# Kernel optimization log

Hardware: AMD Instinct MI355X
Metric: run time of the kernel (lower is better)

## Reference

```python
import jax, jax.numpy as jnp
import numpy as np

B, L, C, H = 256, 200, 4, 128


def setup_inputs() -> dict:
    key = jax.random.key(0)
    ks = jax.random.split(key, 6)
    seqs = jax.random.normal(ks[0], (B, L, C, H), dtype=jnp.float32)
    # valid prefix of random length, padding (True) at the tail
    lengths = jax.random.randint(ks[1], (B,), 1, L + 1)
    timeline_mask = (jnp.arange(L)[None, :] >= lengths[:, None])[:, :, None]  # [B,L,1] bool
    attention_mask = jnp.zeros((L, L), dtype=bool)  # unused by the module
    s = 1.0 / np.sqrt(H)  # torch GRU default init U(-1/sqrt(H), 1/sqrt(H))
    W_ih = jax.random.uniform(ks[2], (C, 3 * H, H), minval=-s, maxval=s, dtype=jnp.float32)
    W_hh = jax.random.uniform(ks[3], (C, 3 * H, H), minval=-s, maxval=s, dtype=jnp.float32)
    b_ih = jax.random.uniform(ks[4], (C, 3 * H), minval=-s, maxval=s, dtype=jnp.float32)
    b_hh = jax.random.uniform(ks[5], (C, 3 * H), minval=-s, maxval=s, dtype=jnp.float32)
    return {"seqs": seqs, "timeline_mask": timeline_mask, "attention_mask": attention_mask,
            "W_ih": W_ih, "W_hh": W_hh, "b_ih": b_ih, "b_hh": b_hh}


def batched_roll(x, shifts):
    # x: [B, L, H]; per-sample circular shift along time (torch.roll semantics)
    Ldim = x.shape[1]
    idx = (jnp.arange(Ldim)[None, :] - shifts[:, None]) % Ldim  # [B, L]
    return jnp.take_along_axis(x, idx[:, :, None], axis=1)


def gru(x, W_ih, W_hh, b_ih, b_hh):
    # single-layer batch_first GRU, h0 = 0 (torch nn.GRU math)
    xp = jnp.einsum('blh,gh->blg', x, W_ih) + b_ih  # [B, L, 3H] input projections
    Hd = W_hh.shape[1]

    def step(h, xt):
        gh = h @ W_hh.T + b_hh
        i_r, i_z, i_n = jnp.split(xt, 3, axis=-1)
        h_r, h_z, h_n = jnp.split(gh, 3, axis=-1)
        r = jax.nn.sigmoid(i_r + h_r)
        z = jax.nn.sigmoid(i_z + h_z)
        n = jnp.tanh(i_n + r * h_n)
        h_new = (1.0 - z) * n + z * h
        return h_new, h_new

    h0 = jnp.zeros((x.shape[0], Hd), x.dtype)
    _, ys = jax.lax.scan(step, h0, jnp.swapaxes(xp, 0, 1))  # scan over time
    return jnp.swapaxes(ys, 0, 1)  # [B, L, H]


def reference(seqs, timeline_mask, attention_mask, W_ih, W_hh, b_ih, b_hh):
    mask = timeline_mask[:, :, 0]                 # [B, L] True = pad
    length = jnp.sum(~mask, axis=1)               # count of valid steps
    zero_length = jnp.sum(mask, axis=1)           # count of padded steps
    outs = []
    for i in range(seqs.shape[2]):                # loop over C experts (distinct weights)
        x = batched_roll(seqs[:, :, i, :], length)
        y = gru(x, W_ih[i], W_hh[i], b_ih[i], b_hh[i])
        y = batched_roll(y, zero_length)
        y = jnp.where(timeline_mask, 0.0, y)      # masked_fill(timeline_mask, 0.0)
        outs.append(y)
    return jnp.stack(outs, axis=0)  # [C, B, L, H] (list of experts in the original)
```

## Files before the change

kernel.cpp:

```cpp
#include <hip/hip_runtime.h>
#include <hip/hip_bf16.h>

#define BB 256
#define LL 200
#define CC 4
#define HH 128
#define G3 384
#define XPAD 168

typedef short bf16x8 __attribute__((ext_vector_type(8)));
typedef float f32x4 __attribute__((ext_vector_type(4)));

#define MFMA16(a, b, c) __builtin_amdgcn_mfma_f32_16x16x32_bf16((a), (b), (c), 0, 0, 0)

__device__ __forceinline__ short bf16_rne(float x) {
    union { float f; unsigned u; } v; v.f = x;
    unsigned r = v.u + 0x7FFFu + ((v.u >> 16) & 1u);
    return (short)(r >> 16);
}
__device__ __forceinline__ float rcp_(float x) { return __builtin_amdgcn_rcpf(x); }
__device__ __forceinline__ float sigm_(float x) { return rcp_(1.0f + __expf(-x)); }
__device__ __forceinline__ float tanhf_(float x) { return 2.0f * rcp_(1.0f + __expf(-2.0f * x)) - 1.0f; }

__device__ __forceinline__ unsigned cvtpk(float lo, float hi) {
    unsigned r;
    asm("v_cvt_pk_bf16_f32 %0, %1, %2" : "=v"(r) : "v"(lo), "v"(hi));
    return r;
}
__device__ __forceinline__ uint2 pack4(float4 v) {
    uint2 p;
    p.x = cvtpk(v.x, v.y);
    p.y = cvtpk(v.z, v.w);
    return p;
}

__global__ void compute_lens_kernel(const unsigned char* __restrict__ mask8,
                                    int* __restrict__ lens) {
    __shared__ int bad;
    int b = threadIdx.x;
    if (b == 0) bad = 0;
    __syncthreads();
    int cnt8 = 0, prev = 0, mono = 1;
    for (int t = 0; t < LL; ++t) {
        int v = mask8[b * LL + t] ? 1 : 0;
        cnt8 += (v == 0);
        if (v < prev) mono = 0;
        prev = v;
    }
    if (!mono) atomicAdd(&bad, 1);
    __syncthreads();
    int len;
    if (bad == 0) {
        len = cnt8;
    } else {
        const int* m32 = (const int*)mask8;
        int c = 0;
        for (int t = 0; t < LL; ++t) c += (m32[b * LL + t] == 0);
        len = c;
    }
    if (len < 1) len = 1;
    if (len > LL) len = LL;
    lens[b] = len;
}

__global__ void wsplit_kernel(const float* __restrict__ Wih, const float* __restrict__ Whh,
                              short* __restrict__ wih_hi, short* __restrict__ whh_hi) {
    int i = blockIdx.x * 256 + threadIdx.x;
    wih_hi[i] = bf16_rne(Wih[i]);
    whh_hi[i] = bf16_rne(Whh[i]);
}

__global__ __launch_bounds__(512, 2) void gru_fused_kernel(
    const float* __restrict__ seqs,
    const int*   __restrict__ lens,
    const short* __restrict__ wih_hi,
    const short* __restrict__ whh_hi,
    const float* __restrict__ b_ih,
    const float* __restrict__ b_hh,
    float*       __restrict__ out)
{
    const int bt = blockIdx.x;
    const int c  = blockIdx.y;
    const int bbase = bt * 16;
    const int tid = threadIdx.x;
    const int w = tid >> 6;
    const int l = tid & 63;
    const int l15 = l & 15, g = l >> 4;

    __shared__ __align__(16) short hA[2][16][XPAD];
    __shared__ __align__(16) short xs[2][16][XPAD];

    bf16x8 BH[3][4], WI[3][4];
    #pragma unroll
    for (int q = 0; q < 3; ++q) {
        const int NT = q * 8 + w;
        #pragma unroll
        for (int ks = 0; ks < 4; ++ks) {
            size_t off = (size_t)(c * G3 + NT * 16 + l15) * HH + ks * 32 + g * 8;
            BH[q][ks] = *(const bf16x8*)(whh_hi + off);
            WI[q][ks] = *(const bf16x8*)(wih_hi + off);
        }
    }
    #pragma unroll
    for (int q = 0; q < 3; ++q)
        asm volatile("" : "+a"(BH[q][0]), "+a"(BH[q][1]), "+a"(BH[q][2]), "+a"(BH[q][3]));

    const int bsl = tid >> 5;
    const int bs  = bbase + bsl;
    const int k0s = (tid & 31) * 4;
    const int lenS = lens[bs];
    const float* srow = seqs + ((size_t)bs * LL * CC + c) * HH + k0s;
    int ts0 = LL - lenS;
    int ts1 = ts0 + 1; if (ts1 >= LL) ts1 -= LL;
    float4 xr0 = *(const float4*)(srow + (size_t)ts0 * (CC * HH));
    float4 xr1 = *(const float4*)(srow + (size_t)ts1 * (CC * HH));
    int txs = ts1 + 1; if (txs >= LL) txs -= LL;

    const int col0 = w * 16 + l15;
    const float bRs = b_hh[c * G3 + col0]       + b_ih[c * G3 + col0];
    const float bZs = b_hh[c * G3 + 128 + col0] + b_ih[c * G3 + 128 + col0];
    const float bHN = b_hh[c * G3 + 256 + col0];
    const float bIN = b_ih[c * G3 + 256 + col0];
    const f32x4 cZZ  = (f32x4){0.f, 0.f, 0.f, 0.f};
    const f32x4 cHN4 = (f32x4){bHN, bHN, bHN, bHN};
    const f32x4 cR4  = (f32x4){bRs, bRs, bRs, bRs};
    const f32x4 cZ4  = (f32x4){bZs, bZs, bZs, bZs};
    const f32x4 cN4  = (f32x4){bIN, bIN, bIN, bIN};

    int lenr[4], tcur[4];
    #pragma unroll
    for (int r = 0; r < 4; ++r) {
        lenr[r] = lens[bbase + g * 4 + r];
        tcur[r] = LL - lenr[r];
    }
    float hold[4] = { 0.f, 0.f, 0.f, 0.f };

    for (int i = tid; i < 16 * XPAD / 2; i += 512) ((int*)hA[0])[i] = 0;

    *(uint2*)&xs[0][bsl][k0s] = pack4(xr0);
    *(uint2*)&xs[1][bsl][k0s] = pack4(xr1);
    __syncthreads();

    f32x4 xacc[3];
    {
        bf16x8 xh0 = *(const bf16x8*)&xs[0][l15][g * 8];
        xacc[0] = MFMA16(xh0, WI[0][0], cR4);
        xacc[1] = MFMA16(xh0, WI[1][0], cZ4);
        xacc[2] = MFMA16(xh0, WI[2][0], cN4);
        #pragma unroll
        for (int ks = 1; ks < 4; ++ks) {
            bf16x8 xh = *(const bf16x8*)&xs[0][l15][ks * 32 + g * 8];
            #pragma unroll
            for (int q = 0; q < 3; ++q)
                xacc[q] = MFMA16(xh, WI[q][ks], xacc[q]);
        }
    }
    float4 xraw = *(const float4*)(srow + (size_t)txs * (CC * HH));
    txs = (txs + 1 == LL) ? 0 : txs + 1;

    __syncthreads();

    for (int si = 0; si < LL; ++si) {
        const int hb = si & 1, hn = hb ^ 1;

        f32x4 racc[3];
        {
            bf16x8 ah0 = *(const bf16x8*)&hA[hb][l15][g * 8];
            racc[0] = MFMA16(ah0, BH[0][0], cZZ);
            racc[1] = MFMA16(ah0, BH[1][0], cZZ);
            racc[2] = MFMA16(ah0, BH[2][0], cHN4);
            #pragma unroll
            for (int ks = 1; ks < 4; ++ks) {
                bf16x8 ah = *(const bf16x8*)&hA[hb][l15][ks * 32 + g * 8];
                #pragma unroll
                for (int q = 0; q < 3; ++q) racc[q] = MFMA16(ah, BH[q][ks], racc[q]);
            }
        }

        float hnew[4];
        #pragma unroll
        for (int r = 0; r < 4; ++r) {
            float gr = sigm_(racc[0][r] + xacc[0][r]);
            float gz = sigm_(racc[1][r] + xacc[1][r]);
            float gn = tanhf_(xacc[2][r] + gr * racc[2][r]);
            float hv = gn + gz * (hold[r] - gn);
            hnew[r] = hv;
            hold[r] = hv;
        }

        {
            unsigned pk01 = cvtpk(hold[0], hold[1]);
            unsigned pk23 = cvtpk(hold[2], hold[3]);
            hA[hn][g * 4 + 0][col0] = (short)(pk01 & 0xffffu);
            hA[hn][g * 4 + 1][col0] = (short)(pk01 >> 16);
            hA[hn][g * 4 + 2][col0] = (short)(pk23 & 0xffffu);
            hA[hn][g * 4 + 3][col0] = (short)(pk23 >> 16);
        }

        #pragma unroll
        for (int r = 0; r < 4; ++r) {
            int t = tcur[r];
            int valid = t < lenr[r];
            out[((size_t)(c * BB + bbase + g * 4 + r) * LL + t) * HH + col0]
                = valid ? hnew[r] : 0.0f;
            tcur[r] = (t + 1 == LL) ? 0 : t + 1;
        }

        {
            bf16x8 xh0 = *(const bf16x8*)&xs[hn][l15][g * 8];
            xacc[0] = MFMA16(xh0, WI[0][0], cR4);
            xacc[1] = MFMA16(xh0, WI[1][0], cZ4);
            xacc[2] = MFMA16(xh0, WI[2][0], cN4);
            #pragma unroll
            for (int ks = 1; ks < 4; ++ks) {
                bf16x8 xh = *(const bf16x8*)&xs[hn][l15][ks * 32 + g * 8];
                #pragma unroll
                for (int q = 0; q < 3; ++q)
                    xacc[q] = MFMA16(xh, WI[q][ks], xacc[q]);
            }
        }

        *(uint2*)&xs[hb][bsl][k0s] = pack4(xraw);
        xraw = *(const float4*)(srow + (size_t)txs * (CC * HH));
        txs = (txs + 1 == LL) ? 0 : txs + 1;

        asm volatile("s_waitcnt lgkmcnt(0)" ::: "memory");
        __builtin_amdgcn_s_barrier();
        __builtin_amdgcn_sched_barrier(0);
        asm volatile("" ::: "memory");
    }
}

extern "C" void kernel_launch(void* const* d_in, const int* in_sizes, int n_in,
                              void* d_out, int out_size, void* d_ws, size_t ws_size,
                              hipStream_t stream) {
    const float* seqs  = (const float*)d_in[0];
    const unsigned char* tmask = (const unsigned char*)d_in[1];
    const float* W_ih  = (const float*)d_in[3];
    const float* W_hh  = (const float*)d_in[4];
    const float* b_ih  = (const float*)d_in[5];
    const float* b_hh  = (const float*)d_in[6];
    float* out = (float*)d_out;

    char* ws = (char*)d_ws;
    int*   lens   = (int*)(ws);
    short* wih_hi = (short*)(ws + 1024);
    short* whh_hi = (short*)(ws + 1024 + 393216);

    compute_lens_kernel<<<1, BB, 0, stream>>>(tmask, lens);
    wsplit_kernel<<<768, 256, 0, stream>>>(W_ih, W_hh, wih_hi, whh_hi);

    gru_fused_kernel<<<dim3(16, CC), 512, 0, stream>>>(
        seqs, lens, wih_hi, whh_hi, b_ih, b_hh, out);
}
```

Baseline: 203.6 us.

## Specialize warps into recurrent and input-projection roles with LDS handoff

```diff
diff --git a/kernel.cpp b/kernel.cpp
--- a/kernel.cpp
+++ b/kernel.cpp
@@ -26,12 +26,6 @@
     unsigned r;
     asm("v_cvt_pk_bf16_f32 %0, %1, %2" : "=v"(r) : "v"(lo), "v"(hi));
     return r;
-}
-__device__ __forceinline__ uint2 pack4(float4 v) {
-    uint2 p;
-    p.x = cvtpk(v.x, v.y);
-    p.y = cvtpk(v.z, v.w);
-    return p;
 }
 
 __global__ void compute_lens_kernel(const unsigned char* __restrict__ mask8,
@@ -86,144 +80,211 @@
     const int w = tid >> 6;
     const int l = tid & 63;
     const int l15 = l & 15, g = l >> 4;
+    const int role = w >> 2;
+    const int wq = w & 3;
 
     __shared__ __align__(16) short hA[2][16][XPAD];
     __shared__ __align__(16) short xs[2][16][XPAD];
-
-    bf16x8 BH[3][4], WI[3][4];
+    __shared__ __align__(16) float xp[G3][16];
+
+    bf16x8 W[6][4];
+    {
+        const short* wsrc = role ? wih_hi : whh_hi;
+        #pragma unroll
+        for (int q = 0; q < 6; ++q) {
+            const int NT = (q >> 1) * 8 + 2 * wq + (q & 1);
+            #pragma unroll
+            for (int ks = 0; ks < 4; ++ks) {
+                size_t off = (size_t)(c * G3 + NT * 16 + l15) * HH + ks * 32 + g * 8;
+                W[q][ks] = *(const bf16x8*)(wsrc + off);
+            }
+        }
+    }
     #pragma unroll
-    for (int q = 0; q < 3; ++q) {
-        const int NT = q * 8 + w;
-        #pragma unroll
-        for (int ks = 0; ks < 4; ++ks) {
-            size_t off = (size_t)(c * G3 + NT * 16 + l15) * HH + ks * 32 + g * 8;
-            BH[q][ks] = *(const bf16x8*)(whh_hi + off);
-            WI[q][ks] = *(const bf16x8*)(wih_hi + off);
-        }
-    }
-    #pragma unroll
-    for (int q = 0; q < 3; ++q)
-        asm volatile("" : "+a"(BH[q][0]), "+a"(BH[q][1]), "+a"(BH[q][2]), "+a"(BH[q][3]));
-
-    const int bsl = tid >> 5;
-    const int bs  = bbase + bsl;
-    const int k0s = (tid & 31) * 4;
-    const int lenS = lens[bs];
-    const float* srow = seqs + ((size_t)bs * LL * CC + c) * HH + k0s;
-    int ts0 = LL - lenS;
-    int ts1 = ts0 + 1; if (ts1 >= LL) ts1 -= LL;
-    float4 xr0 = *(const float4*)(srow + (size_t)ts0 * (CC * HH));
-    float4 xr1 = *(const float4*)(srow + (size_t)ts1 * (CC * HH));
-    int txs = ts1 + 1; if (txs >= LL) txs -= LL;
-
-    const int col0 = w * 16 + l15;
-    const float bRs = b_hh[c * G3 + col0]       + b_ih[c * G3 + col0];
-    const float bZs = b_hh[c * G3 + 128 + col0] + b_ih[c * G3 + 128 + col0];
-    const float bHN = b_hh[c * G3 + 256 + col0];
-    const float bIN = b_ih[c * G3 + 256 + col0];
-    const f32x4 cZZ  = (f32x4){0.f, 0.f, 0.f, 0.f};
-    const f32x4 cHN4 = (f32x4){bHN, bHN, bHN, bHN};
-    const f32x4 cR4  = (f32x4){bRs, bRs, bRs, bRs};
-    const f32x4 cZ4  = (f32x4){bZs, bZs, bZs, bZs};
-    const f32x4 cN4  = (f32x4){bIN, bIN, bIN, bIN};
+    for (int q = 0; q < 6; ++q)
+        asm volatile("" : "+a"(W[q][0]), "+a"(W[q][1]), "+a"(W[q][2]), "+a"(W[q][3]));
+
+    const int colA = 32 * wq + l15;
+    const int colB = colA + 16;
+
+    f32x4 ci[6];
+    if (role) {
+        float bRa = b_hh[c * G3 + colA]       + b_ih[c * G3 + colA];
+        float bRb = b_hh[c * G3 + colB]       + b_ih[c * G3 + colB];
+        float bZa = b_hh[c * G3 + 128 + colA] + b_ih[c * G3 + 128 + colA];
+        float bZb = b_hh[c * G3 + 128 + colB] + b_ih[c * G3 + 128 + colB];
+        float bNa = b_ih[c * G3 + 256 + colA];
+        float bNb = b_ih[c * G3 + 256 + colB];
+        ci[0] = (f32x4){bRa, bRa, bRa, bRa};
+        ci[1] = (f32x4){bRb, bRb, bRb, bRb};
+        ci[2] = (f32x4){bZa, bZa, bZa, bZa};
+        ci[3] = (f32x4){bZb, bZb, bZb, bZb};
+        ci[4] = (f32x4){bNa, bNa, bNa, bNa};
+        ci[5] = (f32x4){bNb, bNb, bNb, bNb};
+    } else {
+        float bHa = b_hh[c * G3 + 256 + colA];
+        float bHb = b_hh[c * G3 + 256 + colB];
+        ci[0] = (f32x4){0.f, 0.f, 0.f, 0.f};
+        ci[1] = (f32x4){0.f, 0.f, 0.f, 0.f};
+        ci[2] = (f32x4){0.f, 0.f, 0.f, 0.f};
+        ci[3] = (f32x4){0.f, 0.f, 0.f, 0.f};
+        ci[4] = (f32x4){bHa, bHa, bHa, bHa};
+        ci[5] = (f32x4){bHb, bHb, bHb, bHb};
+    }
 
     int lenr[4], tcur[4];
-    #pragma unroll
-    for (int r = 0; r < 4; ++r) {
-        lenr[r] = lens[bbase + g * 4 + r];
-        tcur[r] = LL - lenr[r];
-    }
-    float hold[4] = { 0.f, 0.f, 0.f, 0.f };
+    float hold[2][4];
+    if (!role) {
+        #pragma unroll
+        for (int r = 0; r < 4; ++r) {
+            lenr[r] = lens[bbase + g * 4 + r];
+            tcur[r] = LL - lenr[r];
+        }
+        #pragma unroll
+        for (int cp = 0; cp < 2; ++cp)
+            #pragma unroll
+            for (int r = 0; r < 4; ++r) hold[cp][r] = 0.f;
+    }
+
+    const int ptid = tid & 255;
+    const int prow = ptid >> 4;
+    const int pk0  = (ptid & 15) * 8;
+    const float* srow = nullptr;
+    float4 xra, xrb;
+    int txs = 0;
+    if (role) {
+        const int lenS = lens[bbase + prow];
+        srow = seqs + ((size_t)(bbase + prow) * LL * CC + c) * HH + pk0;
+        int t0 = LL - lenS;
+        int t1 = t0 + 1; if (t1 >= LL) t1 -= LL;
+        float4 a0 = *(const float4*)(srow + (size_t)t0 * (CC * HH));
+        float4 a1 = *(const float4*)(srow + (size_t)t0 * (CC * HH) + 4);
+        float4 b0 = *(const float4*)(srow + (size_t)t1 * (CC * HH));
+        float4 b1 = *(const float4*)(srow + (size_t)t1 * (CC * HH) + 4);
+        *(uint4*)&xs[0][prow][pk0] = make_uint4(cvtpk(a0.x, a0.y), cvtpk(a0.z, a0.w),
+                                                cvtpk(a1.x, a1.y), cvtpk(a1.z, a1.w));
+        *(uint4*)&xs[1][prow][pk0] = make_uint4(cvtpk(b0.x, b0.y), cvtpk(b0.z, b0.w),
+                                                cvtpk(b1.x, b1.y), cvtpk(b1.z, b1.w));
+        txs = t1 + 1; if (txs >= LL) txs -= LL;
+        xra = *(const float4*)(srow + (size_t)txs * (CC * HH));
+        xrb = *(const float4*)(srow + (size_t)txs * (CC * HH) + 4);
+        txs = (txs + 1 == LL) ? 0 : txs + 1;
+    }
 
     for (int i = tid; i < 16 * XPAD / 2; i += 512) ((int*)hA[0])[i] = 0;
-
-    *(uint2*)&xs[0][bsl][k0s] = pack4(xr0);
-    *(uint2*)&xs[1][bsl][k0s] = pack4(xr1);
     __syncthreads();
 
-    f32x4 xacc[3];
-    {
-        bf16x8 xh0 = *(const bf16x8*)&xs[0][l15][g * 8];
-        xacc[0] = MFMA16(xh0, WI[0][0], cR4);
-        xacc[1] = MFMA16(xh0, WI[1][0], cZ4);
-        xacc[2] = MFMA16(xh0, WI[2][0], cN4);
-        #pragma unroll
-        for (int ks = 1; ks < 4; ++ks) {
-            bf16x8 xh = *(const bf16x8*)&xs[0][l15][ks * 32 + g * 8];
-            #pragma unroll
-            for (int q = 0; q < 3; ++q)
-                xacc[q] = MFMA16(xh, WI[q][ks], xacc[q]);
-        }
-    }
-    float4 xraw = *(const float4*)(srow + (size_t)txs * (CC * HH));
-    txs = (txs + 1 == LL) ? 0 : txs + 1;
-
+    if (role) {
+        bf16x8 xh[4];
+        #pragma unroll
+        for (int ks = 0; ks < 4; ++ks)
+            xh[ks] = *(const bf16x8*)&xs[0][l15][ks * 32 + g * 8];
+        f32x4 xn[6];
+        #pragma unroll
+        for (int q = 0; q < 6; ++q) xn[q] = ci[q];
+        #pragma unroll
+        for (int ks = 0; ks < 4; ++ks)
+            #pragma unroll
+            for (int q = 0; q < 6; ++q)
+                xn[q] = MFMA16(xh[ks], W[q][ks], xn[q]);
+        #pragma unroll
+        for (int q = 0; q < 6; ++q) {
+            const int NT = (q >> 1) * 8 + 2 * wq + (q & 1);
+            *(f32x4*)&xp[NT * 16 + l15][g * 4] = xn[q];
+        }
+    }
     __syncthreads();
 
     for (int si = 0; si < LL; ++si) {
         const int hb = si & 1, hn = hb ^ 1;
 
-        f32x4 racc[3];
-        {
-            bf16x8 ah0 = *(const bf16x8*)&hA[hb][l15][g * 8];
-            racc[0] = MFMA16(ah0, BH[0][0], cZZ);
-            racc[1] = MFMA16(ah0, BH[1][0], cZZ);
-            racc[2] = MFMA16(ah0, BH[2][0], cHN4);
-            #pragma unroll
-            for (int ks = 1; ks < 4; ++ks) {
-                bf16x8 ah = *(const bf16x8*)&hA[hb][l15][ks * 32 + g * 8];
+        bf16x8 ah[4], xh[4];
+        f32x4 xpv[6];
+        if (!role) {
+            #pragma unroll
+            for (int ks = 0; ks < 4; ++ks)
+                ah[ks] = *(const bf16x8*)&hA[hb][l15][ks * 32 + g * 8];
+            #pragma unroll
+            for (int q = 0; q < 6; ++q) {
+                const int NT = (q >> 1) * 8 + 2 * wq + (q & 1);
+                xpv[q] = *(const f32x4*)&xp[NT * 16 + l15][g * 4];
+            }
+        } else {
+            #pragma unroll
+            for (int ks = 0; ks < 4; ++ks)
+                xh[ks] = *(const bf16x8*)&xs[hn][l15][ks * 32 + g * 8];
+        }
+        asm volatile("s_waitcnt lgkmcnt(0)" ::: "memory");
+        __builtin_amdgcn_s_barrier();
+        __builtin_amdgcn_sched_barrier(0);
+
+        if (!role) {
+            f32x4 racc[6];
+            #pragma unroll
+            for (int q = 0; q < 6; ++q) racc[q] = ci[q];
+            #pragma unroll
+            for (int ks = 0; ks < 4; ++ks)
                 #pragma unroll
-                for (int q = 0; q < 3; ++q) racc[q] = MFMA16(ah, BH[q][ks], racc[q]);
-            }
-        }
-
-        float hnew[4];
-        #pragma unroll
-        for (int r = 0; r < 4; ++r) {
-            float gr = sigm_(racc[0][r] + xacc[0][r]);
-            float gz = sigm_(racc[1][r] + xacc[1][r]);
-            float gn = tanhf_(xacc[2][r] + gr * racc[2][r]);
-            float hv = gn + gz * (hold[r] - gn);
-            hnew[r] = hv;
-            hold[r] = hv;
-        }
-
-        {
-            unsigned pk01 = cvtpk(hold[0], hold[1]);
-            unsigned pk23 = cvtpk(hold[2], hold[3]);
-            hA[hn][g * 4 + 0][col0] = (short)(pk01 & 0xffffu);
-            hA[hn][g * 4 + 1][col0] = (short)(pk01 >> 16);
-            hA[hn][g * 4 + 2][col0] = (short)(pk23 & 0xffffu);
-            hA[hn][g * 4 + 3][col0] = (short)(pk23 >> 16);
-        }
-
-        #pragma unroll
-        for (int r = 0; r < 4; ++r) {
-            int t = tcur[r];
-            int valid = t < lenr[r];
-            out[((size_t)(c * BB + bbase + g * 4 + r) * LL + t) * HH + col0]
-                = valid ? hnew[r] : 0.0f;
-            tcur[r] = (t + 1 == LL) ? 0 : t + 1;
-        }
-
-        {
-            bf16x8 xh0 = *(const bf16x8*)&xs[hn][l15][g * 8];
-            xacc[0] = MFMA16(xh0, WI[0][0], cR4);
-            xacc[1] = MFMA16(xh0, WI[1][0], cZ4);
-            xacc[2] = MFMA16(xh0, WI[2][0], cN4);
-            #pragma unroll
-            for (int ks = 1; ks < 4; ++ks) {
-                bf16x8 xh = *(const bf16x8*)&xs[hn][l15][ks * 32 + g * 8];
+                for (int q = 0; q < 6; ++q)
+                    racc[q] = MFMA16(ah[ks], W[q][ks], racc[q]);
+
+            float hnew[2][4];
+            #pragma unroll
+            for (int cp = 0; cp < 2; ++cp)
                 #pragma unroll
-                for (int q = 0; q < 3; ++q)
-                    xacc[q] = MFMA16(xh, WI[q][ks], xacc[q]);
-            }
-        }
-
-        *(uint2*)&xs[hb][bsl][k0s] = pack4(xraw);
-        xraw = *(const float4*)(srow + (size_t)txs * (CC * HH));
-        txs = (txs + 1 == LL) ? 0 : txs + 1;
-
+                for (int r = 0; r < 4; ++r) {
+                    float gr = sigm_(racc[0 + cp][r] + xpv[0 + cp][r]);
+                    float gz = sigm_(racc[2 + cp][r] + xpv[2 + cp][r]);
+                    float gn = tanhf_(xpv[4 + cp][r] + gr * racc[4 + cp][r]);
+                    float hv = gn + gz * (hold[cp][r] - gn);
+                    hnew[cp][r] = hv;
+                    hold[cp][r] = hv;
+                }
+
+            {
+                unsigned pA01 = cvtpk(hold[0][0], hold[0][1]);
+                unsigned pA23 = cvtpk(hold[0][2], hold[0][3]);
+                unsigned pB01 = cvtpk(hold[1][0], hold[1][1]);
+                unsigned pB23 = cvtpk(hold[1][2], hold[1][3]);
+                hA[hn][g * 4 + 0][colA] = (short)(pA01 & 0xffffu);
+                hA[hn][g * 4 + 1][colA] = (short)(pA01 >> 16);
+                hA[hn][g * 4 + 2][colA] = (short)(pA23 & 0xffffu);
+                hA[hn][g * 4 + 3][colA] = (short)(pA23 >> 16);
+                hA[hn][g * 4 + 0][colB] = (short)(pB01 & 0xffffu);
+                hA[hn][g * 4 + 1][colB] = (short)(pB01 >> 16);
+                hA[hn][g * 4 + 2][colB] = (short)(pB23 & 0xffffu);
+                hA[hn][g * 4 + 3][colB] = (short)(pB23 >> 16);
+            }
+
+            #pragma unroll
+            for (int r = 0; r < 4; ++r) {
+                int t = tcur[r];
+                int valid = t < lenr[r];
+                float* op = &out[((size_t)(c * BB + bbase + g * 4 + r) * LL + t) * HH + colA];
+                op[0]  = valid ? hnew[0][r] : 0.0f;
+                op[16] = valid ? hnew[1][r] : 0.0f;
+                tcur[r] = (t + 1 == LL) ? 0 : t + 1;
+            }
+        } else {
+            f32x4 xn[6];
+            #pragma unroll
+            for (int q = 0; q < 6; ++q) xn[q] = ci[q];
+            #pragma unroll
+            for (int ks = 0; ks < 4; ++ks)
+                #pragma unroll
+                for (int q = 0; q < 6; ++q)
+                    xn[q] = MFMA16(xh[ks], W[q][ks], xn[q]);
+            #pragma unroll
+            for (int q = 0; q < 6; ++q) {
+                const int NT = (q >> 1) * 8 + 2 * wq + (q & 1);
+                *(f32x4*)&xp[NT * 16 + l15][g * 4] = xn[q];
+            }
+            *(uint4*)&xs[hb][prow][pk0] = make_uint4(cvtpk(xra.x, xra.y), cvtpk(xra.z, xra.w),
+                                                     cvtpk(xrb.x, xrb.y), cvtpk(xrb.z, xrb.w));
+            xra = *(const float4*)(srow + (size_t)txs * (CC * HH));
+            xrb = *(const float4*)(srow + (size_t)txs * (CC * HH) + 4);
+            txs = (txs + 1 == LL) ? 0 : txs + 1;
+        }
         asm volatile("s_waitcnt lgkmcnt(0)" ::: "memory");
         __builtin_amdgcn_s_barrier();
         __builtin_amdgcn_sched_barrier(0);
```

New measurement: 280.2 us. +37.6%, slower.

## Store h and x tiles in MFMA fragment order and strength-reduce global pointers

Applied to the files above, without the earlier changes.

```diff
diff --git a/kernel.cpp b/kernel.cpp
--- a/kernel.cpp
+++ b/kernel.cpp
@@ -6,7 +6,6 @@
 #define CC 4
 #define HH 128
 #define G3 384
-#define XPAD 168
 
 typedef short bf16x8 __attribute__((ext_vector_type(8)));
 typedef float f32x4 __attribute__((ext_vector_type(4)));
@@ -87,8 +86,8 @@
     const int l = tid & 63;
     const int l15 = l & 15, g = l >> 4;
 
-    __shared__ __align__(16) short hA[2][16][XPAD];
-    __shared__ __align__(16) short xs[2][16][XPAD];
+    __shared__ __align__(16) short hA[2][4][512];
+    __shared__ __align__(16) short xs[2][4][512];
 
     bf16x8 BH[3][4], WI[3][4];
     #pragma unroll
@@ -101,22 +100,26 @@
             WI[q][ks] = *(const bf16x8*)(wih_hi + off);
         }
     }
-    #pragma unroll
-    for (int q = 0; q < 3; ++q)
-        asm volatile("" : "+a"(BH[q][0]), "+a"(BH[q][1]), "+a"(BH[q][2]), "+a"(BH[q][3]));
+
+    const int col0 = w * 16 + l15;
+    const int ksw = w >> 1;
+    const int hwbase = (((w & 1) * 2 + (l15 >> 3)) * 16 + g * 4) * 8 + (l15 & 7);
 
     const int bsl = tid >> 5;
-    const int bs  = bbase + bsl;
     const int k0s = (tid & 31) * 4;
-    const int lenS = lens[bs];
-    const float* srow = seqs + ((size_t)bs * LL * CC + c) * HH + k0s;
+    const int ksx = k0s >> 5;
+    const int xwbase = ((((k0s >> 3) & 3) * 16 + bsl) * 8 + (k0s & 7));
+    const int lenS = lens[bbase + bsl];
+    const float* srow0 = seqs + ((size_t)(bbase + bsl) * LL * CC + c) * HH + k0s;
     int ts0 = LL - lenS;
     int ts1 = ts0 + 1; if (ts1 >= LL) ts1 -= LL;
-    float4 xr0 = *(const float4*)(srow + (size_t)ts0 * (CC * HH));
-    float4 xr1 = *(const float4*)(srow + (size_t)ts1 * (CC * HH));
+    float4 xr0 = *(const float4*)(srow0 + (size_t)ts0 * (CC * HH));
+    float4 xr1 = *(const float4*)(srow0 + (size_t)ts1 * (CC * HH));
     int txs = ts1 + 1; if (txs >= LL) txs -= LL;
-
-    const int col0 = w * 16 + l15;
+    const float* xptr = srow0 + (size_t)txs * (CC * HH);
+    const ptrdiff_t xstep = CC * HH;
+    const ptrdiff_t xwrap = (ptrdiff_t)(LL - 1) * CC * HH;
+
     const float bRs = b_hh[c * G3 + col0]       + b_ih[c * G3 + col0];
     const float bZs = b_hh[c * G3 + 128 + col0] + b_ih[c * G3 + 128 + col0];
     const float bHN = b_hh[c * G3 + 256 + col0];
@@ -128,35 +131,39 @@
     const f32x4 cN4  = (f32x4){bIN, bIN, bIN, bIN};
 
     int lenr[4], tcur[4];
+    float* optr[4];
     #pragma unroll
     for (int r = 0; r < 4; ++r) {
         lenr[r] = lens[bbase + g * 4 + r];
         tcur[r] = LL - lenr[r];
-    }
+        optr[r] = out + ((size_t)(c * BB + bbase + g * 4 + r) * LL + tcur[r]) * HH + col0;
+    }
+    const ptrdiff_t owrap = (ptrdiff_t)(LL - 1) * HH;
     float hold[4] = { 0.f, 0.f, 0.f, 0.f };
 
-    for (int i = tid; i < 16 * XPAD / 2; i += 512) ((int*)hA[0])[i] = 0;
-
-    *(uint2*)&xs[0][bsl][k0s] = pack4(xr0);
-    *(uint2*)&xs[1][bsl][k0s] = pack4(xr1);
+    for (int i = tid; i < 1024; i += 512) ((int*)hA[0])[i] = 0;
+
+    *(uint2*)&xs[0][ksx][xwbase] = pack4(xr0);
+    *(uint2*)&xs[1][ksx][xwbase] = pack4(xr1);
     __syncthreads();
 
     f32x4 xacc[3];
     {
-        bf16x8 xh0 = *(const bf16x8*)&xs[0][l15][g * 8];
+        bf16x8 xh0 = *(const bf16x8*)&xs[0][0][l * 8];
         xacc[0] = MFMA16(xh0, WI[0][0], cR4);
         xacc[1] = MFMA16(xh0, WI[1][0], cZ4);
         xacc[2] = MFMA16(xh0, WI[2][0], cN4);
         #pragma unroll
         for (int ks = 1; ks < 4; ++ks) {
-            bf16x8 xh = *(const bf16x8*)&xs[0][l15][ks * 32 + g * 8];
+            bf16x8 xh = *(const bf16x8*)&xs[0][ks][l * 8];
             #pragma unroll
             for (int q = 0; q < 3; ++q)
                 xacc[q] = MFMA16(xh, WI[q][ks], xacc[q]);
         }
     }
-    float4 xraw = *(const float4*)(srow + (size_t)txs * (CC * HH));
+    float4 xraw = *(const float4*)xptr;
     txs = (txs + 1 == LL) ? 0 : txs + 1;
+    xptr = (txs == 0) ? xptr - xwrap : xptr + xstep;
 
     __syncthreads();
 
@@ -165,13 +172,13 @@
 
         f32x4 racc[3];
         {
-            bf16x8 ah0 = *(const bf16x8*)&hA[hb][l15][g * 8];
+            bf16x8 ah0 = *(const bf16x8*)&hA[hb][0][l * 8];
             racc[0] = MFMA16(ah0, BH[0][0], cZZ);
             racc[1] = MFMA16(ah0, BH[1][0], cZZ);
             racc[2] = MFMA16(ah0, BH[2][0], cHN4);
             #pragma unroll
             for (int ks = 1; ks < 4; ++ks) {
-                bf16x8 ah = *(const bf16x8*)&hA[hb][l15][ks * 32 + g * 8];
+                bf16x8 ah = *(const bf16x8*)&hA[hb][ks][l * 8];
                 #pragma unroll
                 for (int q = 0; q < 3; ++q) racc[q] = MFMA16(ah, BH[q][ks], racc[q]);
             }
@@ -191,38 +198,39 @@
         {
             unsigned pk01 = cvtpk(hold[0], hold[1]);
             unsigned pk23 = cvtpk(hold[2], hold[3]);
-            hA[hn][g * 4 + 0][col0] = (short)(pk01 & 0xffffu);
-            hA[hn][g * 4 + 1][col0] = (short)(pk01 >> 16);
-            hA[hn][g * 4 + 2][col0] = (short)(pk23 & 0xffffu);
-            hA[hn][g * 4 + 3][col0] = (short)(pk23 >> 16);
+            hA[hn][ksw][hwbase]      = (short)(pk01 & 0xffffu);
+            hA[hn][ksw][hwbase + 8]  = (short)(pk01 >> 16);
+            hA[hn][ksw][hwbase + 16] = (short)(pk23 & 0xffffu);
+            hA[hn][ksw][hwbase + 24] = (short)(pk23 >> 16);
         }
 
         #pragma unroll
         for (int r = 0; r < 4; ++r) {
             int t = tcur[r];
-            int valid = t < lenr[r];
-            out[((size_t)(c * BB + bbase + g * 4 + r) * LL + t) * HH + col0]
-                = valid ? hnew[r] : 0.0f;
-            tcur[r] = (t + 1 == LL) ? 0 : t + 1;
+            *optr[r] = (t < lenr[r]) ? hnew[r] : 0.0f;
+            int wrapped = (t + 1 == LL);
+            tcur[r] = wrapped ? 0 : t + 1;
+            optr[r] = wrapped ? optr[r] - owrap : optr[r] + HH;
         }
 
         {
-            bf16x8 xh0 = *(const bf16x8*)&xs[hn][l15][g * 8];
+            bf16x8 xh0 = *(const bf16x8*)&xs[hn][0][l * 8];
             xacc[0] = MFMA16(xh0, WI[0][0], cR4);
             xacc[1] = MFMA16(xh0, WI[1][0], cZ4);
             xacc[2] = MFMA16(xh0, WI[2][0], cN4);
             #pragma unroll
             for (int ks = 1; ks < 4; ++ks) {
-                bf16x8 xh = *(const bf16x8*)&xs[hn][l15][ks * 32 + g * 8];
+                bf16x8 xh = *(const bf16x8*)&xs[hn][ks][l * 8];
                 #pragma unroll
                 for (int q = 0; q < 3; ++q)
                     xacc[q] = MFMA16(xh, WI[q][ks], xacc[q]);
             }
         }
 
-        *(uint2*)&xs[hb][bsl][k0s] = pack4(xraw);
-        xraw = *(const float4*)(srow + (size_t)txs * (CC * HH));
+        *(uint2*)&xs[hb][ksx][xwbase] = pack4(xraw);
+        xraw = *(const float4*)xptr;
         txs = (txs + 1 == LL) ? 0 : txs + 1;
+        xptr = (txs == 0) ? xptr - xwrap : xptr + xstep;
 
         asm volatile("s_waitcnt lgkmcnt(0)" ::: "memory");
         __builtin_amdgcn_s_barrier();
```

After: 203.8 us. About the same (+0.1%).
